# Optimization experiments

Measured on AMD Instinct MI355X. Metric: run time of the kernel, lower is better.

## Reference

```python
import jax, jax.numpy as jnp
import numpy as np

WS = (7, 7, 7)          # (Wz, Wh, Ww)
NUM_HEADS = 3


def rel_position_index(ws):
    # Faithful to meshgrid_3d in the source: arrays are reversed, grid i varies
    # along axis i, so coords are stacked in (w, h, z) order.
    wz, wh, ww = ws
    g = np.meshgrid(np.arange(ww), np.arange(wh), np.arange(wz), indexing='ij')
    coords = np.stack(g)                      # (3, ww, wh, wz)
    flat = coords.reshape(3, -1)              # (3, N)
    rel = flat[:, :, None] - flat[:, None, :]  # (3, N, N)
    rel = rel.transpose(1, 2, 0).astype(np.int64)  # (N, N, 3)
    rel[:, :, 0] += wz - 1
    rel[:, :, 1] += wh - 1
    rel[:, :, 2] += ww - 1
    rel[:, :, 0] *= (2 * wh - 1) * (2 * ww - 1)
    rel[:, :, 1] *= (2 * ww - 1)
    return rel.sum(-1)                        # (N, N) in [0, (2W-1)^3)


REL_IDX = jnp.asarray(rel_position_index(WS).reshape(-1), dtype=jnp.int32)


def setup_inputs() -> dict:
    key = jax.random.key(0)
    ks = jax.random.split(key, 6)
    B, N, C = 256, 343, 96
    nW = 32
    x = jax.random.normal(ks[0], (B, N, C), dtype=jnp.float32)
    # shifted-window mask: 0 where attendable, -100 where blocked
    keep = jax.random.uniform(ks[1], (nW, N, N)) < 0.9
    mask = jnp.where(keep, 0.0, -100.0).astype(jnp.float32)
    w_qkv = jax.random.normal(ks[2], (C, 3 * C), dtype=jnp.float32) * 0.05
    b_qkv = jnp.zeros((3 * C,), jnp.float32)
    bias_table = jax.random.normal(ks[3], (2197, NUM_HEADS), dtype=jnp.float32) * 0.02
    w_proj = jax.random.normal(ks[4], (C, C), dtype=jnp.float32) * 0.05
    b_proj = jnp.zeros((C,), jnp.float32)
    return {"x": x, "mask": mask, "w_qkv": w_qkv, "b_qkv": b_qkv,
            "bias_table": bias_table, "w_proj": w_proj, "b_proj": b_proj}


def reference(x, mask, w_qkv, b_qkv, bias_table, w_proj, b_proj):
    B, N, C = x.shape
    H = NUM_HEADS
    hd = C // H
    scale = hd ** -0.5  # qk_scale is None -> head_dim**-0.5 (swin v1 path)
    # QKV projection, split to heads: (3, B, H, N, hd)
    qkv = (x @ w_qkv + b_qkv).reshape(B, N, 3, H, hd).transpose(2, 0, 3, 1, 4)
    q, k, v = qkv[0] * scale, qkv[1], qkv[2]
    attn = jnp.einsum('bhnd,bhmd->bhnm', q, k)        # (B, H, N, N)
    # gathered relative-position bias -> (H, N, N)
    bias = bias_table[REL_IDX].reshape(N, N, H).transpose(2, 0, 1)
    attn = attn + bias[None]
    # shifted-window mask add: reshape to (B//nW, nW, H, N, N)
    nW = mask.shape[0]
    attn = attn.reshape(B // nW, nW, H, N, N) + mask[None, :, None]
    attn = jax.nn.softmax(attn.reshape(B, H, N, N), axis=-1)
    out = jnp.einsum('bhnm,bhmd->bhnd', attn, v)      # (B, H, N, hd)
    out = out.transpose(0, 2, 1, 3).reshape(B, N, C)
    return out @ w_proj + b_proj
```

## Files before the change

kernel.cpp:

```cpp
#include <hip/hip_runtime.h>

#define N_TOK 343
#define NP 352
#define C_DIM 96
#define HEADS 3
#define HD 32
#define B_SZ 256
#define NW 32
#define QKV_COLS 288

#define QKV_ELEMS (B_SZ * HEADS * N_TOK * HD)
#define X2_ELEMS ((long)B_SZ * N_TOK * C_DIM)
#define CMB_ELEMS ((long)NW * HEADS * N_TOK * NP)

typedef _Float16 f16;
typedef _Float16 f16x2 __attribute__((ext_vector_type(2)));
typedef _Float16 f16x4 __attribute__((ext_vector_type(4)));
typedef _Float16 f16x8 __attribute__((ext_vector_type(8)));
typedef float f32x4 __attribute__((ext_vector_type(4)));

__global__ __launch_bounds__(256) void wprep_kernel(
    const float* __restrict__ w_qkv, const float* __restrict__ w_proj,
    f16* __restrict__ wt_qkv, f16* __restrict__ wt_proj) {
  const int e = blockIdx.x * 256 + threadIdx.x;
  if (e < QKV_COLS * 96) {
    const int cc = e / 96, k = e % 96;
    wt_qkv[e] = (f16)w_qkv[k * QKV_COLS + cc];
  } else {
    const int e2 = e - QKV_COLS * 96;
    if (e2 < 96 * 96) {
      const int cc = e2 / 96, k = e2 % 96;
      wt_proj[e2] = (f16)w_proj[k * 96 + cc];
    }
  }
}

__global__ __launch_bounds__(384) void cmb_kernel(
    const float* __restrict__ mask, const float* __restrict__ bias_table,
    f16* __restrict__ cmb) {
  const int q = blockIdx.x;
  const int w = blockIdx.y;
  const int key = threadIdx.x;
  if (key >= NP) return;
  const int bn = (q / 49) * 169 + ((q / 7) % 7) * 13 + (q % 7);
  const float LOG2E = 1.4426950408889634f;
  float mv = 0.f;
  int idx = 0;
  const bool valid = (key < N_TOK);
  if (valid) {
    const int bm = (key / 49) * 169 + ((key / 7) % 7) * 13 + (key % 7);
    idx = (bn - bm + 1098) * HEADS;
    mv = mask[((long)w * N_TOK + q) * N_TOK + key];
  }
#pragma unroll
  for (int h = 0; h < HEADS; ++h) {
    const float val = valid ? (bias_table[idx + h] + mv) * LOG2E : -14427.0f;
    cmb[((long)(w * HEADS + h) * N_TOK + q) * NP + key] = (f16)val;
  }
}

__global__ __launch_bounds__(256) void qkv_mfma_kernel(
    const float* __restrict__ x, const f16* __restrict__ wt,
    const float* __restrict__ bias,
    f16* __restrict__ Q, f16* __restrict__ K, f16* __restrict__ V) {
  __shared__ f16 sh[4][16][40];
  const int tid = threadIdx.x;
  const int wave = tid >> 6, lane = tid & 63;
  const int c = lane & 15, g = lane >> 4;
  const long rowTile = (long)blockIdx.x * 64 + wave * 16;
  const long arow = rowTile + c;

  f16x8 af[3];
#pragma unroll
  for (int ks = 0; ks < 3; ++ks) {
    const float* px = x + arow * 96 + ks * 32 + g * 8;
    const float4 lo = *(const float4*)px;
    const float4 hi = *(const float4*)(px + 4);
    f16x8 v;
    v[0] = (f16)lo.x; v[1] = (f16)lo.y; v[2] = (f16)lo.z; v[3] = (f16)lo.w;
    v[4] = (f16)hi.x; v[5] = (f16)hi.y; v[6] = (f16)hi.z; v[7] = (f16)hi.w;
    af[ks] = v;
  }

  const int rowL = (int)rowTile + (lane >> 2);
  const int bL = rowL / N_TOK, nL = rowL % N_TOK;

  const f32x4 zero = {0.f, 0.f, 0.f, 0.f};
  const float scale = 0.17677669529663687f * 1.4426950408889634f;

#pragma unroll
  for (int p = 0; p < 9; ++p) {
    const int which = p / 3;
    const int h = p % 3;
    const float mult = (which == 0) ? scale : 1.0f;
#pragma unroll
    for (int e = 0; e < 2; ++e) {
      const int ct = 2 * p + e;
      f32x4 acc = zero;
#pragma unroll
      for (int ks = 0; ks < 3; ++ks) {
        const f16x8 bf = *(const f16x8*)(wt + (ct * 16 + c) * 96 + ks * 32 + g * 8);
        acc = __builtin_amdgcn_mfma_f32_16x16x32_f16(af[ks], bf, acc, 0, 0, 0);
      }
      const float bv = bias[ct * 16 + c];
#pragma unroll
      for (int r = 0; r < 4; ++r)
        sh[wave][4 * g + r][(e << 4) + c] = (f16)((acc[r] + bv) * mult);
    }
    __builtin_amdgcn_wave_barrier();
    const f16x8 po = *(const f16x8*)&sh[wave][lane >> 2][(lane & 3) * 8];
    __builtin_amdgcn_wave_barrier();
    f16* dst = (which == 0) ? Q : (which == 1) ? K : V;
    *(f16x8*)(dst + (((long)bL * HEADS + h) * N_TOK + nL) * HD + (lane & 3) * 8) = po;
  }
}

__global__ __launch_bounds__(256) void attn_kernel(
    const f16* __restrict__ Qh, const f16* __restrict__ Kh,
    const f16* __restrict__ Vh, const f16* __restrict__ CMB,
    f16* __restrict__ X2h) {
  __shared__ f16 Ks[NP][40];
  __shared__ f16 Vt[HD][356];

  const int blk = blockIdx.x;
  const int b = blk / HEADS;
  const int h = blk % HEADS;
  const int tid = threadIdx.x;
  const int wave = tid >> 6;
  const int lane = tid & 63;
  const int c = lane & 15;
  const int g = lane >> 4;

  const f16* Kg = Kh + (long)blk * (N_TOK * HD);
  const f16* Vg = Vh + (long)blk * (N_TOK * HD);
  const f16* Qg = Qh + (long)blk * (N_TOK * HD);

  for (int u = tid; u < NP * 4; u += 256) {
    const int key = u >> 2, j = u & 3;
    f16x8 val = {0, 0, 0, 0, 0, 0, 0, 0};
    if (key < N_TOK) val = *(const f16x8*)(Kg + key * HD + j * 8);
    *(f16x8*)&Ks[key][j * 8] = val;
  }
  for (int i = tid; i < N_TOK * 16; i += 256) {
    const int n = i >> 4, dp = i & 15;
    const f16x2 v2 = *(const f16x2*)(Vg + n * HD + dp * 2);
    Vt[2 * dp][n] = v2.x;
    Vt[2 * dp + 1][n] = v2.y;
  }
  for (int i = tid; i < HD * 13; i += 256) Vt[i / 13][N_TOK + i % 13] = (f16)0;
  __syncthreads();

  const int w = b & (NW - 1);
  const f32x4 zero = {0.f, 0.f, 0.f, 0.f};

  for (int qt = wave; qt < NP / 16; qt += 4) {
    const int q = qt * 16 + c;
    const int qrow = (q < N_TOK) ? q : (N_TOK - 1);
    const f16x8 qf = *(const f16x8*)(Qg + qrow * HD + g * 8);
    const f16* cmrow = CMB + ((long)(w * HEADS + h) * N_TOK + qrow) * NP;

    f32x4 acc0 = zero, acc1 = zero;
    float lsum = 0.f;

    f16x4 cm0 = *(const f16x4*)(cmrow + 4 * g);
    f16x4 cm1 = *(const f16x4*)(cmrow + 16 + 4 * g);

    for (int kt = 0; kt < NP / 32; ++kt) {
      f16x4 ncm0, ncm1;
      if (kt < NP / 32 - 1) {
        ncm0 = *(const f16x4*)(cmrow + 32 * (kt + 1) + 4 * g);
        ncm1 = *(const f16x4*)(cmrow + 32 * (kt + 1) + 16 + 4 * g);
      }
      const f16x8 kf0 = *(const f16x8*)&Ks[32 * kt + c][g * 8];
      const f16x8 kf1 = *(const f16x8*)&Ks[32 * kt + 16 + c][g * 8];

      const f32x4 s0 = __builtin_amdgcn_mfma_f32_16x16x32_f16(kf0, qf, zero, 0, 0, 0);
      const f32x4 s1 = __builtin_amdgcn_mfma_f32_16x16x32_f16(kf1, qf, zero, 0, 0, 0);

      float p0[4], p1[4];
#pragma unroll
      for (int r = 0; r < 4; ++r) {
        p0[r] = __builtin_amdgcn_exp2f(s0[r] + (float)cm0[r]);
        p1[r] = __builtin_amdgcn_exp2f(s1[r] + (float)cm1[r]);
        lsum += p0[r] + p1[r];
      }
      const f16x2 a0 = __builtin_bit_cast(f16x2, __builtin_amdgcn_cvt_pkrtz(p0[0], p0[1]));
      const f16x2 a1 = __builtin_bit_cast(f16x2, __builtin_amdgcn_cvt_pkrtz(p0[2], p0[3]));
      const f16x2 a2 = __builtin_bit_cast(f16x2, __builtin_amdgcn_cvt_pkrtz(p1[0], p1[1]));
      const f16x2 a3 = __builtin_bit_cast(f16x2, __builtin_amdgcn_cvt_pkrtz(p1[2], p1[3]));
      const f16x4 plo = __builtin_shufflevector(a0, a1, 0, 1, 2, 3);
      const f16x4 phi = __builtin_shufflevector(a2, a3, 0, 1, 2, 3);
      const f16x8 pf = __builtin_shufflevector(plo, phi, 0, 1, 2, 3, 4, 5, 6, 7);

      const f16x4 va0 = *(const f16x4*)&Vt[c][32 * kt + 4 * g];
      const f16x4 va1 = *(const f16x4*)&Vt[c][32 * kt + 16 + 4 * g];
      const f16x4 vb0 = *(const f16x4*)&Vt[16 + c][32 * kt + 4 * g];
      const f16x4 vb1 = *(const f16x4*)&Vt[16 + c][32 * kt + 16 + 4 * g];
      const f16x8 vf0 = __builtin_shufflevector(va0, va1, 0, 1, 2, 3, 4, 5, 6, 7);
      const f16x8 vf1 = __builtin_shufflevector(vb0, vb1, 0, 1, 2, 3, 4, 5, 6, 7);

      acc0 = __builtin_amdgcn_mfma_f32_16x16x32_f16(vf0, pf, acc0, 0, 0, 0);
      acc1 = __builtin_amdgcn_mfma_f32_16x16x32_f16(vf1, pf, acc1, 0, 0, 0);

      cm0 = ncm0;
      cm1 = ncm1;
    }

    lsum += __shfl_xor(lsum, 16);
    lsum += __shfl_xor(lsum, 32);
    const float inv = 1.f / lsum;

    if (q < N_TOK) {
      f16* orow = X2h + ((long)b * N_TOK + q) * C_DIM + h * HD;
      f16x4 o0, o1;
#pragma unroll
      for (int r = 0; r < 4; ++r) {
        o0[r] = (f16)(acc0[r] * inv);
        o1[r] = (f16)(acc1[r] * inv);
      }
      *(f16x4*)(orow + 4 * g) = o0;
      *(f16x4*)(orow + 16 + 4 * g) = o1;
    }
  }
}

__global__ __launch_bounds__(256) void proj_mfma_kernel(
    const f16* __restrict__ X2h, const f16* __restrict__ wt,
    const float* __restrict__ bias, float* __restrict__ out) {
  __shared__ float shp[4][16][100];
  const int tid = threadIdx.x;
  const int wave = tid >> 6, lane = tid & 63;
  const int c = lane & 15, g = lane >> 4;
  const long rowTile = (long)blockIdx.x * 64 + wave * 16;
  const long arow = rowTile + c;

  f16x8 af[3];
#pragma unroll
  for (int ks = 0; ks < 3; ++ks)
    af[ks] = *(const f16x8*)(X2h + arow * 96 + ks * 32 + g * 8);

  const f32x4 zero = {0.f, 0.f, 0.f, 0.f};
#pragma unroll
  for (int ct = 0; ct < 6; ++ct) {
    f32x4 acc = zero;
#pragma unroll
    for (int ks = 0; ks < 3; ++ks) {
      const f16x8 bf = *(const f16x8*)(wt + (ct * 16 + c) * 96 + ks * 32 + g * 8);
      acc = __builtin_amdgcn_mfma_f32_16x16x32_f16(af[ks], bf, acc, 0, 0, 0);
    }
    const float bv = bias[ct * 16 + c];
#pragma unroll
    for (int r = 0; r < 4; ++r)
      shp[wave][4 * g + r][ct * 16 + c] = acc[r] + bv;
  }
  __builtin_amdgcn_wave_barrier();
#pragma unroll
  for (int i = 0; i < 6; ++i) {
    const int u = lane + 64 * i;
    const int row = u / 24, ch = u % 24;
    const float4 v = *(const float4*)&shp[wave][row][ch * 4];
    *(float4*)(out + (rowTile + row) * 96 + ch * 4) = v;
  }
}

extern "C" void kernel_launch(void* const* d_in, const int* in_sizes, int n_in,
                              void* d_out, int out_size, void* d_ws, size_t ws_size,
                              hipStream_t stream) {
  const float* x          = (const float*)d_in[0];
  const float* mask       = (const float*)d_in[1];
  const float* w_qkv      = (const float*)d_in[2];
  const float* b_qkv      = (const float*)d_in[3];
  const float* bias_table = (const float*)d_in[4];
  const float* w_proj     = (const float*)d_in[5];
  const float* b_proj     = (const float*)d_in[6];
  float* out = (float*)d_out;

  f16* Qh = (f16*)d_ws;
  f16* Kh = Qh + QKV_ELEMS;
  f16* Vh = Kh + QKV_ELEMS;
  f16* X2h = Vh + QKV_ELEMS;
  f16* CMB = X2h + X2_ELEMS;
  f16* WTQ = CMB + CMB_ELEMS;
  f16* WTP = WTQ + QKV_COLS * 96;

  const int wBlocks = (QKV_COLS * 96 + 96 * 96 + 255) / 256;
  const int gemmBlocks = (B_SZ * N_TOK) / 64;

  wprep_kernel<<<wBlocks, 256, 0, stream>>>(w_qkv, w_proj, WTQ, WTP);
  cmb_kernel<<<dim3(N_TOK, NW), 384, 0, stream>>>(mask, bias_table, CMB);
  qkv_mfma_kernel<<<gemmBlocks, 256, 0, stream>>>(x, WTQ, b_qkv, Qh, Kh, Vh);
  attn_kernel<<<B_SZ * HEADS, 256, 0, stream>>>(Qh, Kh, Vh, CMB, X2h);
  proj_mfma_kernel<<<gemmBlocks, 256, 0, stream>>>(X2h, WTP, b_proj, out);
}
```

Before: 200.6 us.

## Stage GEMM weights in LDS and preload all mask-bias tiles in attention

The QKV and projection GEMM kernels now copy the transposed fp16 weights into padded shared memory once per block and read B fragments from LDS instead of global memory. The QKV kernel also grows to 512 threads and 128 rows per block, so each weight copy is shared by more rows. In the attention kernel, all 11 combined mask/bias fragments for a query tile are loaded into registers before a fully unrolled key loop, replacing the one-step-ahead prefetch. The trade-offs are extra LDS use and a block-wide sync in the GEMMs, plus higher register pressure in attention that may lower occupancy.

```diff
diff --git a/kernel.cpp b/kernel.cpp
--- a/kernel.cpp
+++ b/kernel.cpp
@@ -8,10 +8,12 @@
 #define B_SZ 256
 #define NW 32
 #define QKV_COLS 288
+#define NKT 11
 
 #define QKV_ELEMS (B_SZ * HEADS * N_TOK * HD)
 #define X2_ELEMS ((long)B_SZ * N_TOK * C_DIM)
 #define CMB_ELEMS ((long)NW * HEADS * N_TOK * NP)
+#define WT_PITCH 104
 
 typedef _Float16 f16;
 typedef _Float16 f16x2 __attribute__((ext_vector_type(2)));
@@ -59,16 +61,22 @@
   }
 }
 
-__global__ __launch_bounds__(256) void qkv_mfma_kernel(
+__global__ __launch_bounds__(512) void qkv_mfma_kernel(
     const float* __restrict__ x, const f16* __restrict__ wt,
     const float* __restrict__ bias,
     f16* __restrict__ Q, f16* __restrict__ K, f16* __restrict__ V) {
-  __shared__ f16 sh[4][16][40];
+  __shared__ f16 wtL[QKV_COLS][WT_PITCH];
+  __shared__ f16 sh[8][16][40];
   const int tid = threadIdx.x;
   const int wave = tid >> 6, lane = tid & 63;
   const int c = lane & 15, g = lane >> 4;
-  const long rowTile = (long)blockIdx.x * 64 + wave * 16;
+  const long rowTile = (long)blockIdx.x * 128 + wave * 16;
   const long arow = rowTile + c;
+
+  for (int u = tid; u < QKV_COLS * 12; u += 512) {
+    const int r = u / 12, ch = u % 12;
+    *(f16x8*)&wtL[r][ch * 8] = *(const f16x8*)(wt + r * 96 + ch * 8);
+  }
 
   f16x8 af[3];
 #pragma unroll
@@ -81,6 +89,7 @@
     v[4] = (f16)hi.x; v[5] = (f16)hi.y; v[6] = (f16)hi.z; v[7] = (f16)hi.w;
     af[ks] = v;
   }
+  __syncthreads();
 
   const int rowL = (int)rowTile + (lane >> 2);
   const int bL = rowL / N_TOK, nL = rowL % N_TOK;
@@ -99,7 +108,7 @@
       f32x4 acc = zero;
 #pragma unroll
       for (int ks = 0; ks < 3; ++ks) {
-        const f16x8 bf = *(const f16x8*)(wt + (ct * 16 + c) * 96 + ks * 32 + g * 8);
+        const f16x8 bf = *(const f16x8*)&wtL[ct * 16 + c][ks * 32 + g * 8];
         acc = __builtin_amdgcn_mfma_f32_16x16x32_f16(af[ks], bf, acc, 0, 0, 0);
       }
       const float bv = bias[ct * 16 + c];
@@ -156,21 +165,21 @@
   for (int qt = wave; qt < NP / 16; qt += 4) {
     const int q = qt * 16 + c;
     const int qrow = (q < N_TOK) ? q : (N_TOK - 1);
+    const f16* cmrow = CMB + ((long)(w * HEADS + h) * N_TOK + qrow) * NP;
+
+    f16x4 cmA[NKT], cmB[NKT];
+#pragma unroll
+    for (int kt = 0; kt < NKT; ++kt) {
+      cmA[kt] = *(const f16x4*)(cmrow + 32 * kt + 4 * g);
+      cmB[kt] = *(const f16x4*)(cmrow + 32 * kt + 16 + 4 * g);
+    }
     const f16x8 qf = *(const f16x8*)(Qg + qrow * HD + g * 8);
-    const f16* cmrow = CMB + ((long)(w * HEADS + h) * N_TOK + qrow) * NP;
 
     f32x4 acc0 = zero, acc1 = zero;
     float lsum = 0.f;
 
-    f16x4 cm0 = *(const f16x4*)(cmrow + 4 * g);
-    f16x4 cm1 = *(const f16x4*)(cmrow + 16 + 4 * g);
-
-    for (int kt = 0; kt < NP / 32; ++kt) {
-      f16x4 ncm0, ncm1;
-      if (kt < NP / 32 - 1) {
-        ncm0 = *(const f16x4*)(cmrow + 32 * (kt + 1) + 4 * g);
-        ncm1 = *(const f16x4*)(cmrow + 32 * (kt + 1) + 16 + 4 * g);
-      }
+#pragma unroll
+    for (int kt = 0; kt < NKT; ++kt) {
       const f16x8 kf0 = *(const f16x8*)&Ks[32 * kt + c][g * 8];
       const f16x8 kf1 = *(const f16x8*)&Ks[32 * kt + 16 + c][g * 8];
 
@@ -180,8 +189,8 @@
       float p0[4], p1[4];
 #pragma unroll
       for (int r = 0; r < 4; ++r) {
-        p0[r] = __builtin_amdgcn_exp2f(s0[r] + (float)cm0[r]);
-        p1[r] = __builtin_amdgcn_exp2f(s1[r] + (float)cm1[r]);
+        p0[r] = __builtin_amdgcn_exp2f(s0[r] + (float)cmA[kt][r]);
+        p1[r] = __builtin_amdgcn_exp2f(s1[r] + (float)cmB[kt][r]);
         lsum += p0[r] + p1[r];
       }
       const f16x2 a0 = __builtin_bit_cast(f16x2, __builtin_amdgcn_cvt_pkrtz(p0[0], p0[1]));
@@ -201,9 +210,6 @@
 
       acc0 = __builtin_amdgcn_mfma_f32_16x16x32_f16(vf0, pf, acc0, 0, 0, 0);
       acc1 = __builtin_amdgcn_mfma_f32_16x16x32_f16(vf1, pf, acc1, 0, 0, 0);
-
-      cm0 = ncm0;
-      cm1 = ncm1;
     }
 
     lsum += __shfl_xor(lsum, 16);
@@ -227,6 +233,7 @@
 __global__ __launch_bounds__(256) void proj_mfma_kernel(
     const f16* __restrict__ X2h, const f16* __restrict__ wt,
     const float* __restrict__ bias, float* __restrict__ out) {
+  __shared__ f16 wtL[C_DIM][WT_PITCH];
   __shared__ float shp[4][16][100];
   const int tid = threadIdx.x;
   const int wave = tid >> 6, lane = tid & 63;
@@ -234,10 +241,16 @@
   const long rowTile = (long)blockIdx.x * 64 + wave * 16;
   const long arow = rowTile + c;
 
+  for (int u = tid; u < C_DIM * 12; u += 256) {
+    const int r = u / 12, ch = u % 12;
+    *(f16x8*)&wtL[r][ch * 8] = *(const f16x8*)(wt + r * 96 + ch * 8);
+  }
+
   f16x8 af[3];
 #pragma unroll
   for (int ks = 0; ks < 3; ++ks)
     af[ks] = *(const f16x8*)(X2h + arow * 96 + ks * 32 + g * 8);
+  __syncthreads();
 
   const f32x4 zero = {0.f, 0.f, 0.f, 0.f};
 #pragma unroll
@@ -245,7 +258,7 @@
     f32x4 acc = zero;
 #pragma unroll
     for (int ks = 0; ks < 3; ++ks) {
-      const f16x8 bf = *(const f16x8*)(wt + (ct * 16 + c) * 96 + ks * 32 + g * 8);
+      const f16x8 bf = *(const f16x8*)&wtL[ct * 16 + c][ks * 32 + g * 8];
       acc = __builtin_amdgcn_mfma_f32_16x16x32_f16(af[ks], bf, acc, 0, 0, 0);
     }
     const float bv = bias[ct * 16 + c];
@@ -284,11 +297,12 @@
   f16* WTP = WTQ + QKV_COLS * 96;
 
   const int wBlocks = (QKV_COLS * 96 + 96 * 96 + 255) / 256;
-  const int gemmBlocks = (B_SZ * N_TOK) / 64;
+  const int qkvBlocks = (B_SZ * N_TOK) / 128;
+  const int projBlocks = (B_SZ * N_TOK) / 64;
 
   wprep_kernel<<<wBlocks, 256, 0, stream>>>(w_qkv, w_proj, WTQ, WTP);
   cmb_kernel<<<dim3(N_TOK, NW), 384, 0, stream>>>(mask, bias_table, CMB);
-  qkv_mfma_kernel<<<gemmBlocks, 256, 0, stream>>>(x, WTQ, b_qkv, Qh, Kh, Vh);
+  qkv_mfma_kernel<<<qkvBlocks, 512, 0, stream>>>(x, WTQ, b_qkv, Qh, Kh, Vh);
   attn_kernel<<<B_SZ * HEADS, 256, 0, stream>>>(Qh, Kh, Vh, CMB, X2h);
-  proj_mfma_kernel<<<gemmBlocks, 256, 0, stream>>>(X2h, WTP, b_proj, out);
-}
+  proj_mfma_kernel<<<projBlocks, 256, 0, stream>>>(X2h, WTP, b_proj, out);
+}
```

Result: no change. 200.2 us (-0.2%).
